# Performance work log

Measured on AMD Instinct MI355X. Metric: run time of the kernel, lower is better.

The kernel has to match this reference:

```python
import jax, jax.numpy as jnp
import numpy as np

HEADS = 20
SHIFT = 0.6931471805599453  # style_alignment_score_shift = log(2)
KEY_SCALE = 1.0             # style_alignment_score_scale
EPS = 1e-5


def expand_first(feat, scale=1.0):
    # feat: [B, H, S, D]; broadcast style features (batch items 0 and B//2)
    b = feat.shape[0]
    fs = jnp.stack([feat[0], feat[b // 2]])[:, None]           # [2,1,H,S,D]
    fs = jnp.broadcast_to(fs, (2, b // 2) + feat.shape[1:])    # [2,B/2,H,S,D]
    if scale != 1:
        fs = jnp.concatenate([fs[:, :1], scale * fs[:, 1:]], axis=1)
    return fs.reshape(feat.shape)


def concat_first(feat, scale=1.0):
    # concatenate style features along the sequence axis (-2)
    return jnp.concatenate([feat, expand_first(feat, scale=scale)], axis=-2)


def adain(feat):
    # stats over sequence axis (-2); torch .var() is unbiased (ddof=1)
    mean = feat.mean(axis=-2, keepdims=True)
    std = jnp.sqrt(feat.var(axis=-2, keepdims=True, ddof=1) + EPS)
    sm = expand_first(mean)
    ss = expand_first(std)
    return (feat - mean) / std * ss + sm


def setup_inputs() -> dict:
    key = jax.random.key(0)
    ks = jax.random.split(key, 6)
    B, S, C = 4, 1024, 1280
    sc = 1.0 / np.sqrt(C)
    return {
        "hidden_states": jax.random.normal(ks[0], (B, S, C), jnp.float32),
        "Wq": jax.random.normal(ks[1], (C, C), jnp.float32) * sc,
        "Wk": jax.random.normal(ks[2], (C, C), jnp.float32) * sc,
        "Wv": jax.random.normal(ks[3], (C, C), jnp.float32) * sc,
        "Wo": jax.random.normal(ks[4], (C, C), jnp.float32) * sc,
        "bo": jnp.zeros((C,), jnp.float32),
    }


def reference(hidden_states, Wq, Wk, Wv, Wo, bo):
    B, S, C = hidden_states.shape
    H = HEADS
    hd = C // H
    scale = hd ** -0.5

    def to_heads(t):  # [B,S,C] -> [B,H,S,hd]
        return t.reshape(B, S, H, hd).transpose(0, 2, 1, 3)

    q = to_heads(hidden_states @ Wq.T)
    k = to_heads(hidden_states @ Wk.T)
    v = to_heads(hidden_states @ Wv.T)

    q = adain(q)              # adain_queries
    k = adain(k)              # adain_keys
    # adain_values = False

    k = concat_first(k, scale=KEY_SCALE)   # [B,H,2S,hd]
    v = concat_first(v)                    # [B,H,2S,hd]

    # shifted scaled dot-product attention (shift added to shared-key block)
    logits = jnp.einsum('bhqd,bhkd->bhqk', q, k) * scale  # [B,H,S,2S]
    bias = jnp.where(jnp.arange(k.shape[-2]) >= S, jnp.float32(SHIFT), jnp.float32(0.0))
    probs = jax.nn.softmax(logits + bias, axis=-1)
    out = jnp.einsum('bhqk,bhkd->bhqd', probs, v)         # [B,H,S,hd]

    out = out.transpose(0, 2, 1, 3).reshape(B, S, C)
    out = out @ Wo.T + bo
    return out
```

## Files before the change

### kernel.cpp

```cpp
#include <hip/hip_runtime.h>
#include <math.h>


typedef __bf16 bf16x8 __attribute__((ext_vector_type(8)));
typedef __bf16 bf16x2_t __attribute__((ext_vector_type(2)));
typedef float f32x4 __attribute__((ext_vector_type(4)));
typedef unsigned short u16x8 __attribute__((ext_vector_type(8)));

#define BDIM 256

__device__ inline unsigned short f2bf(float f) {
  return __builtin_bit_cast(unsigned short, (__bf16)f);
}
__device__ inline unsigned int pack_bf2(float lo, float hi) {
  bf16x2_t v;
  v[0] = (__bf16)lo;
  v[1] = (__bf16)hi;
  return __builtin_bit_cast(unsigned int, v);
}
__device__ inline float bf2f(unsigned short h) {
  return __uint_as_float(((unsigned int)h) << 16);
}

__device__ inline void gl_lds16(const unsigned short* g, unsigned short* l) {
  __builtin_amdgcn_global_load_lds(
      (const __attribute__((address_space(1))) unsigned int*)g,
      (__attribute__((address_space(3))) unsigned int*)l, 16, 0, 0);
}

__global__ __launch_bounds__(BDIM) void k_convert_all(
    const float* __restrict__ X, const float* __restrict__ Wq,
    const float* __restrict__ Wk, const float* __restrict__ Wv,
    const float* __restrict__ Wo, unsigned short* __restrict__ Xbf,
    unsigned short* __restrict__ Wcat, unsigned short* __restrict__ Wobf) {
  const int idx = blockIdx.x * BDIM + threadIdx.x;
  const float* src;
  unsigned short* dst;
  int off;
  if (idx < 1310720) {
    src = X; dst = Xbf; off = idx;
  } else {
    const int r = idx - 1310720;
    const int which = r / 409600;
    off = r - which * 409600;
    src = (which == 0) ? Wq : (which == 1) ? Wk : (which == 2) ? Wv : Wo;
    dst = (which < 3) ? Wcat + (size_t)which * 1638400 : Wobf;
  }
  const float4 v = ((const float4*)src)[off];
  ushort4 o;
  o.x = f2bf(v.x); o.y = f2bf(v.y); o.z = f2bf(v.z); o.w = f2bf(v.w);
  ((ushort4*)dst)[off] = o;
}

__global__ __launch_bounds__(512, 1) void k_gemm_bf16(
    const unsigned short* __restrict__ A, const unsigned short* __restrict__ B,
    unsigned short* __restrict__ Cbf, int M, int N, int K) {
  __shared__ unsigned short lds[2][2][16384];

  const int bid = blockIdx.x;
  const int swz = (bid & 7) * 30 + (bid >> 3);
  const int mt = swz & 15, nt = swz >> 4;
  const int mBase = mt * 256, nBase = nt * 256;

  const int t = threadIdx.x;
  const int w = t >> 6, lane = t & 63, quad = lane >> 4, l16 = lane & 15;
  const int wrow = w & 1, wcol = w >> 1;
  const int glg = (lane & 7) ^ ((lane >> 3) & 7);
  const int NTILES = K >> 6;

  f32x4 acc[8][4];
#pragma unroll
  for (int i = 0; i < 8; ++i)
#pragma unroll
    for (int j = 0; j < 4; ++j) acc[i][j] = (f32x4){0.f, 0.f, 0.f, 0.f};

  auto stage = [&](int s, int kt) {
#pragma unroll
    for (int j = 0; j < 4; ++j) {
      const int row = j * 64 + w * 8 + (lane >> 3);
      gl_lds16(A + (size_t)(mBase + row) * K + kt * 64 + glg * 8,
               &lds[s][0][(j * 512 + w * 64 + lane) * 8]);
    }
#pragma unroll
    for (int j = 0; j < 4; ++j) {
      const int row = j * 64 + w * 8 + (lane >> 3);
      gl_lds16(B + (size_t)(nBase + row) * K + kt * 64 + glg * 8,
               &lds[s][1][(j * 512 + w * 64 + lane) * 8]);
    }
  };

  stage(0, 0);
  stage(1, 1);
  asm volatile("s_waitcnt vmcnt(8)" ::: "memory");
  __builtin_amdgcn_s_barrier();

  const int arow0 = (wrow * 128 + l16) * 64;
  const int brow0 = (wcol * 64 + l16) * 64;
  const int g0 = ((quad) ^ (l16 & 7)) * 8;
  const int g1 = ((4 + quad) ^ (l16 & 7)) * 8;

  for (int kt = 0; kt < NTILES; ++kt) {
    const int s = kt & 1;
    if (kt >= 1 && kt + 1 < NTILES) stage(s ^ 1, kt + 1);
    const unsigned short* As = &lds[s][0][0];
    const unsigned short* Bs = &lds[s][1][0];
#pragma unroll
    for (int ph = 0; ph < 4; ++ph) {
      const int mh = ph >> 1, nh = ph & 1;
      bf16x8 af[4][2], bq[2][2];
#pragma unroll
      for (int mi = 0; mi < 4; ++mi) {
        const int ro = arow0 + (mh * 4 + mi) * 1024;
        af[mi][0] = *(const bf16x8*)(As + ro + g0);
        af[mi][1] = *(const bf16x8*)(As + ro + g1);
      }
#pragma unroll
      for (int ni = 0; ni < 2; ++ni) {
        const int ro = brow0 + (nh * 2 + ni) * 1024;
        bq[ni][0] = *(const bf16x8*)(Bs + ro + g0);
        bq[ni][1] = *(const bf16x8*)(Bs + ro + g1);
      }
      __builtin_amdgcn_s_setprio(1);
#pragma unroll
      for (int kk = 0; kk < 2; ++kk)
#pragma unroll
        for (int mi = 0; mi < 4; ++mi)
#pragma unroll
          for (int ni = 0; ni < 2; ++ni)
            acc[mh * 4 + mi][nh * 2 + ni] =
                __builtin_amdgcn_mfma_f32_16x16x32_bf16(
                    af[mi][kk], bq[ni][kk], acc[mh * 4 + mi][nh * 2 + ni], 0,
                    0, 0);
      __builtin_amdgcn_s_setprio(0);
      if (ph < 3) __builtin_amdgcn_s_barrier();
    }
    asm volatile("s_waitcnt vmcnt(0)" ::: "memory");
    __builtin_amdgcn_s_barrier();
  }

#pragma unroll
  for (int mi = 0; mi < 8; ++mi)
#pragma unroll
    for (int r = 0; r < 4; ++r) {
      const int row = mBase + wrow * 128 + mi * 16 + quad * 4 + r;
#pragma unroll
      for (int ni = 0; ni < 4; ++ni)
        Cbf[(size_t)row * N + nBase + wcol * 64 + ni * 16 + l16] =
            f2bf(acc[mi][ni][r]);
    }
}

__global__ __launch_bounds__(BDIM, 2) void k_gemm_out(
    const unsigned short* __restrict__ A, const unsigned short* __restrict__ B,
    float* __restrict__ Cf, const float* __restrict__ bias, int M, int N,
    int K) {
  __shared__ unsigned short lds[2][2][8192];

  const int bid = blockIdx.x;
  const int swz = (bid & 7) * 40 + (bid >> 3);
  const int mt = swz & 31, nt = swz >> 5;
  const int mBase = mt * 128, nBase = nt * 128;

  const int t = threadIdx.x;
  const int w = t >> 6, lane = t & 63, quad = lane >> 4, l16 = lane & 15;
  const int wrow = w & 1, wcol = w >> 1;
  const int glg = (lane & 7) ^ ((lane >> 3) & 7);
  const int NTILES = K >> 6;

  f32x4 acc[4][4];
#pragma unroll
  for (int i = 0; i < 4; ++i)
#pragma unroll
    for (int j = 0; j < 4; ++j) acc[i][j] = (f32x4){0.f, 0.f, 0.f, 0.f};

  auto stage = [&](int s, int kt) {
#pragma unroll
    for (int j = 0; j < 4; ++j) {
      const int row = j * 32 + (t >> 3);
      gl_lds16(A + (size_t)(mBase + row) * K + kt * 64 + glg * 8,
               &lds[s][0][(j * 256 + t) * 8]);
    }
#pragma unroll
    for (int j = 0; j < 4; ++j) {
      const int row = j * 32 + (t >> 3);
      gl_lds16(B + (size_t)(nBase + row) * K + kt * 64 + glg * 8,
               &lds[s][1][(j * 256 + t) * 8]);
    }
  };

  stage(0, 0);
  stage(1, 1);
  asm volatile("s_waitcnt vmcnt(8)" ::: "memory");
  __builtin_amdgcn_s_barrier();

  const int arow0 = (wrow * 64 + l16) * 64;
  const int brow0 = (wcol * 64 + l16) * 64;
  const int g0 = ((quad) ^ (l16 & 7)) * 8;
  const int g1 = ((4 + quad) ^ (l16 & 7)) * 8;

  for (int kt = 0; kt < NTILES; ++kt) {
    const int s = kt & 1;
    if (kt >= 1 && kt + 1 < NTILES) stage(s ^ 1, kt + 1);
    const unsigned short* As = &lds[s][0][0];
    const unsigned short* Bs = &lds[s][1][0];
#pragma unroll
    for (int ph = 0; ph < 2; ++ph) {
      bf16x8 af[2][2], bq[4][2];
#pragma unroll
      for (int mi = 0; mi < 2; ++mi) {
        const int ro = arow0 + (ph * 2 + mi) * 1024;
        af[mi][0] = *(const bf16x8*)(As + ro + g0);
        af[mi][1] = *(const bf16x8*)(As + ro + g1);
      }
#pragma unroll
      for (int ni = 0; ni < 4; ++ni) {
        const int ro = brow0 + ni * 1024;
        bq[ni][0] = *(const bf16x8*)(Bs + ro + g0);
        bq[ni][1] = *(const bf16x8*)(Bs + ro + g1);
      }
      __builtin_amdgcn_s_setprio(1);
#pragma unroll
      for (int kk = 0; kk < 2; ++kk)
#pragma unroll
        for (int mi = 0; mi < 2; ++mi)
#pragma unroll
          for (int ni = 0; ni < 4; ++ni)
            acc[ph * 2 + mi][ni] = __builtin_amdgcn_mfma_f32_16x16x32_bf16(
                af[mi][kk], bq[ni][kk], acc[ph * 2 + mi][ni], 0, 0, 0);
      __builtin_amdgcn_s_setprio(0);
      if (ph == 0) __builtin_amdgcn_s_barrier();
    }
    asm volatile("s_waitcnt vmcnt(0)" ::: "memory");
    __builtin_amdgcn_s_barrier();
  }

#pragma unroll
  for (int mi = 0; mi < 4; ++mi)
#pragma unroll
    for (int r = 0; r < 4; ++r) {
      const int row = mBase + wrow * 64 + mi * 16 + quad * 4 + r;
#pragma unroll
      for (int ni = 0; ni < 4; ++ni) {
        const int col = nBase + wcol * 64 + ni * 16 + l16;
        Cf[(size_t)row * N + col] = acc[mi][ni][r] + bias[col];
      }
    }
}

__global__ __launch_bounds__(320) void k_stats1(
    const unsigned short* __restrict__ QKV, float* __restrict__ psum,
    float* __restrict__ psq) {
  const int z = blockIdx.y, which = z >> 2, b = z & 3;
  const int c = threadIdx.x * 4;
  const size_t base =
      (size_t)(b * 1024 + blockIdx.x * 32) * 3840 + which * 1280 + c;
  float4 s = {0.f, 0.f, 0.f, 0.f}, s2 = {0.f, 0.f, 0.f, 0.f};
#pragma unroll 8
  for (int i = 0; i < 32; ++i) {
    const ushort4 xv = *(const ushort4*)(QKV + base + (size_t)i * 3840);
    const float x0 = bf2f(xv.x), x1 = bf2f(xv.y), x2 = bf2f(xv.z),
                x3 = bf2f(xv.w);
    s.x += x0; s.y += x1; s.z += x2; s.w += x3;
    s2.x = fmaf(x0, x0, s2.x); s2.y = fmaf(x1, x1, s2.y);
    s2.z = fmaf(x2, x2, s2.z); s2.w = fmaf(x3, x3, s2.w);
  }
  const size_t o = ((size_t)z * 32 + blockIdx.x) * 1280 + c;
  *(float4*)(psum + o) = s;
  *(float4*)(psq + o) = s2;
}

__global__ __launch_bounds__(BDIM) void k_stats2(
    const float* __restrict__ psum, const float* __restrict__ psq,
    float* __restrict__ fst) {
  const int which = blockIdx.y;
  const int c = blockIdx.x * 256 + threadIdx.x;
  float m[4], sd[4];
#pragma unroll
  for (int b = 0; b < 4; ++b) {
    const int z = which * 4 + b;
    float s = 0.f, s2 = 0.f;
#pragma unroll
    for (int j = 0; j < 32; ++j) {
      s += psum[((size_t)z * 32 + j) * 1280 + c];
      s2 += psq[((size_t)z * 32 + j) * 1280 + c];
    }
    const float mean = s * (1.0f / 1024.0f);
    const float var = (s2 - 1024.0f * mean * mean) * (1.0f / 1023.0f);
    m[b] = mean;
    sd[b] = sqrtf(var + 1e-5f);
  }
  const float S2 = 0.125f * 1.44269504088896341f;
#pragma unroll
  for (int b = 0; b < 4; ++b) {
    const int bs = (b < 2) ? 0 : 2;
    const float g = sd[bs] / sd[b];
    const float o = m[bs] - m[b] * g;
    if (which == 0) {
      fst[(0 * 4 + b) * 1280 + c] = g;
      fst[(1 * 4 + b) * 1280 + c] = o;
    } else {
      fst[(2 * 4 + b) * 1280 + c] = g * S2;
      fst[(3 * 4 + b) * 1280 + c] = o;
    }
  }
}

__global__ __launch_bounds__(BDIM) void k_vt(
    const unsigned short* __restrict__ QKV, unsigned short* __restrict__ vt) {
  __shared__ unsigned short tile[64][65];
  const int tb = blockIdx.x;
  const int b = tb / 320;
  const int r2 = tb - b * 320;
  const int c0 = (r2 / 16) * 64;
  const int s0 = (r2 & 15) * 64;
  const int t = threadIdx.x;
  const int r = t >> 2, seg = (t & 3) * 16;
  const size_t goff = ((size_t)(b * 1024 + s0 + r)) * 3840 + 2560 + c0 + seg;
  const u16x8 va = *(const u16x8*)(QKV + goff);
  const u16x8 vb = *(const u16x8*)(QKV + goff + 8);
#pragma unroll
  for (int j = 0; j < 8; j++) {
    tile[r][seg + j] = va[j];
    tile[r][seg + 8 + j] = vb[j];
  }
  __syncthreads();
  u16x8 o0, o1;
#pragma unroll
  for (int j = 0; j < 8; j++) {
    o0[j] = tile[seg + j][r];
    o1[j] = tile[seg + 8 + j][r];
  }
  const size_t ooff = ((size_t)(b * 1280 + c0 + r)) * 1024 + s0 + seg;
  *(u16x8*)(vt + ooff) = o0;
  *(u16x8*)(vt + ooff + 8) = o1;
}

__global__ __launch_bounds__(BDIM, 4) void k_attn(
    const unsigned short* __restrict__ qkv, const float* __restrict__ fst,
    const unsigned short* __restrict__ vt, unsigned short* __restrict__ Op0,
    unsigned short* __restrict__ Op1, float* __restrict__ Lpart) {
  const int S = 1024;
  const int L = blockIdx.x + 8 * (blockIdx.y + 20 * blockIdx.z);
  const int qt = (L >> 3) & 7;
  const int hz = (L & 7) + ((L >> 6) << 3);
  const int h = hz % 20;
  const int zs = hz / 20;
  int b, chunk;
  if (zs < 2)      { b = 0; chunk = zs; }
  else if (zs < 6) { b = 1; chunk = zs - 2; }
  else if (zs < 8) { b = 2; chunk = zs - 6; }
  else             { b = 3; chunk = zs - 8; }
  const int ktBeg = chunk * 8;
  const int t = threadIdx.x, w = t >> 6, lane = t & 63;
  const int quad = lane >> 4, l16 = lane & 15;
  const int bstyle = (b < 2) ? 0 : 2;
  const int qrow = qt * 128 + w * 32;
  const bool style = (ktBeg >= 16);

  __shared__ unsigned short Ks[2][2][64 * 32];
  __shared__ unsigned short Vs[2][64 * 32];
  __shared__ unsigned short Plds[4][32][64];

  const float S2 = 0.125f * 1.44269504088896341f;

  bf16x8 aq[2][2];
  float biasv[2];
  {
    const int bk = style ? bstyle : b;
    float rq[2] = {0.f, 0.f};
#pragma unroll
    for (int hf = 0; hf < 2; ++hf) {
      const int cc = h * 64 + quad * 8 + hf * 32;
      float gq[8], oq[8], gs[8], ok[8];
      *(float4*)(gq)     = *(const float4*)(fst + (0 * 4 + b) * 1280 + cc);
      *(float4*)(gq + 4) = *(const float4*)(fst + (0 * 4 + b) * 1280 + cc + 4);
      *(float4*)(oq)     = *(const float4*)(fst + (1 * 4 + b) * 1280 + cc);
      *(float4*)(oq + 4) = *(const float4*)(fst + (1 * 4 + b) * 1280 + cc + 4);
      *(float4*)(gs)     = *(const float4*)(fst + (2 * 4 + bk) * 1280 + cc);
      *(float4*)(gs + 4) = *(const float4*)(fst + (2 * 4 + bk) * 1280 + cc + 4);
      *(float4*)(ok)     = *(const float4*)(fst + (3 * 4 + bk) * 1280 + cc);
      *(float4*)(ok + 4) = *(const float4*)(fst + (3 * 4 + bk) * 1280 + cc + 4);
#pragma unroll
      for (int g = 0; g < 2; ++g) {
        const size_t qoff =
            ((size_t)(b * S + qrow + g * 16 + l16)) * 3840 + cc;
        const bf16x8 qv = *(const bf16x8*)(qkv + qoff);
        bf16x8 av;
#pragma unroll
        for (int j = 0; j < 8; ++j) {
          const float qn = fmaf((float)qv[j], gq[j], oq[j]);
          rq[g] = fmaf(qn, ok[j], rq[g]);
          av[j] = (__bf16)(qn * gs[j]);
        }
        aq[g][hf] = av;
      }
    }
    const float shift = style ? 1.0f : 0.0f;
#pragma unroll
    for (int g = 0; g < 2; ++g) {
      float r = rq[g] * S2;
      r += __shfl_xor(r, 16, 64);
      r += __shfl_xor(r, 32, 64);
      biasv[g] = shift + r;
    }
  }

  bf16x8 ones;
#pragma unroll
  for (int i = 0; i < 8; ++i) ones[i] = (__bf16)1.0f;

  f32x4 o[2][4], lsum[2];
#pragma unroll
  for (int g = 0; g < 2; ++g) {
    lsum[g] = (f32x4){0.f, 0.f, 0.f, 0.f};
#pragma unroll
    for (int i = 0; i < 4; i++) o[g][i] = (f32x4){0.f, 0.f, 0.f, 0.f};
  }

  const int krow = t >> 2;
  const int kseg = ((t & 3) ^ ((t >> 3) & 3)) * 8;
  const int sw = l16 & 14;
  const int qsw = (quad ^ ((l16 >> 1) & 3)) * 8;

  auto stageK = [&](int buf, int kt) {
    const int bs = (kt < 16) ? b : bstyle;
    const int sk = (kt & 15) * 64;
    const unsigned short* kg =
        qkv + (size_t)(bs * S + sk + krow) * 3840 + 1280 + h * 64 + kseg;
    gl_lds16(kg, Ks[buf][0] + t * 8);
    gl_lds16(kg + 32, Ks[buf][1] + t * 8);
  };
  auto stageV = [&](int kt) {
    const int bs = (kt < 16) ? b : bstyle;
    const int sk = (kt & 15) * 64;
    const unsigned short* vg =
        vt + (size_t)(bs * 1280 + h * 64 + krow) * S + sk + kseg;
    gl_lds16(vg, Vs[0] + t * 8);
    gl_lds16(vg + 32, Vs[1] + t * 8);
  };

  stageK(0, ktBeg);

  for (int i = 0; i < 8; ++i) {
    const int kt = ktBeg + i;
    const int buf = i & 1;
    asm volatile("s_waitcnt vmcnt(0)" ::: "memory");
    __builtin_amdgcn_s_barrier();
    stageV(kt);
    if (i + 1 < 8) stageK(buf ^ 1, kt + 1);

    f32x4 z2[2][4];
#pragma unroll
    for (int nt = 0; nt < 4; ++nt) {
      const bf16x8 bk0 =
          *(const bf16x8*)(Ks[buf][0] + (nt * 16 + l16) * 32 + qsw);
      const bf16x8 bk1 =
          *(const bf16x8*)(Ks[buf][1] + (nt * 16 + l16) * 32 + qsw);
#pragma unroll
      for (int g = 0; g < 2; ++g) {
        f32x4 zz = (f32x4){0.f, 0.f, 0.f, 0.f};
        zz = __builtin_amdgcn_mfma_f32_16x16x32_bf16(bk0, aq[g][0], zz, 0, 0, 0);
        zz = __builtin_amdgcn_mfma_f32_16x16x32_bf16(bk1, aq[g][1], zz, 0, 0, 0);
        z2[g][nt] = zz;
      }
    }

#pragma unroll
    for (int g = 0; g < 2; ++g) {
      const float bg = biasv[g];
#pragma unroll
      for (int nt = 0; nt < 4; ++nt) {
        const float e0 = exp2f(z2[g][nt][0] + bg);
        const float e1 = exp2f(z2[g][nt][1] + bg);
        const float e2 = exp2f(z2[g][nt][2] + bg);
        const float e3 = exp2f(z2[g][nt][3] + bg);
        uint2 pk;
        pk.x = pack_bf2(e0, e1);
        pk.y = pack_bf2(e2, e3);
        const int phys = (nt * 4 + quad) ^ sw;
        *(uint2*)(&Plds[w][g * 16 + l16][phys * 4]) = pk;
      }
    }

    if (i + 1 < 8)
      asm volatile("s_waitcnt vmcnt(2)" ::: "memory");
    else
      asm volatile("s_waitcnt vmcnt(0)" ::: "memory");
    __builtin_amdgcn_s_barrier();

#pragma unroll
    for (int g = 0; g < 2; ++g) {
      const int a0 = (2 * quad) ^ sw;
      const int a1 = (2 * quad + 8) ^ sw;
      const bf16x8 pa0 = *(const bf16x8*)(&Plds[w][g * 16 + l16][a0 * 4]);
      const bf16x8 pa1 = *(const bf16x8*)(&Plds[w][g * 16 + l16][a1 * 4]);
      lsum[g] = __builtin_amdgcn_mfma_f32_16x16x32_bf16(pa0, ones, lsum[g], 0, 0, 0);
      lsum[g] = __builtin_amdgcn_mfma_f32_16x16x32_bf16(pa1, ones, lsum[g], 0, 0, 0);
#pragma unroll
      for (int dt = 0; dt < 4; ++dt) {
        const bf16x8 vb0 =
            *(const bf16x8*)(Vs[0] + (dt * 16 + l16) * 32 + qsw);
        const bf16x8 vb1 =
            *(const bf16x8*)(Vs[1] + (dt * 16 + l16) * 32 + qsw);
        o[g][dt] =
            __builtin_amdgcn_mfma_f32_16x16x32_bf16(pa0, vb0, o[g][dt], 0, 0, 0);
        o[g][dt] =
            __builtin_amdgcn_mfma_f32_16x16x32_bf16(pa1, vb1, o[g][dt], 0, 0, 0);
      }
    }
  }

  if (l16 == 0) {
#pragma unroll
    for (int g = 0; g < 2; ++g)
#pragma unroll
      for (int r = 0; r < 4; ++r)
        Lpart[((size_t)zs * 20 + h) * 1024 + qrow + g * 16 + quad * 4 + r] =
            lsum[g][r];
  }

  unsigned short* Op = (zs < 4) ? Op0 + (size_t)zs * 1310720
                                : Op1 + (size_t)(zs - 4) * 1310720;
#pragma unroll
  for (int g = 0; g < 2; ++g)
#pragma unroll
    for (int dt = 0; dt < 4; ++dt)
#pragma unroll
      for (int r = 0; r < 4; ++r)
        Op[(size_t)(qrow + g * 16 + quad * 4 + r) * 1280 + h * 64 + dt * 16 +
           l16] = f2bf(o[g][dt][r]);
}

__global__ __launch_bounds__(BDIM) void k_combine(
    const unsigned short* __restrict__ Op0, const unsigned short* __restrict__ Op1,
    const float* __restrict__ Lpart, unsigned short* __restrict__ attnb) {
  const int idx = blockIdx.x * BDIM + threadIdx.x;
  const int row = idx / 160;
  const int c = (idx - row * 160) * 8;
  const int b = row >> 10, q = row & 1023, h = c >> 6;
  const int zb = (b >> 1) * 6 + (b & 1) * 2;
  const int ns = 2 + (b & 1) * 2;
  float L = 0.f;
  float acc[8] = {0.f, 0.f, 0.f, 0.f, 0.f, 0.f, 0.f, 0.f};
  for (int s = 0; s < ns; ++s) {
    const int z = zb + s;
    const unsigned short* base = (z < 4)
        ? Op0 + (size_t)z * 1310720
        : Op1 + (size_t)(z - 4) * 1310720;
    L += Lpart[((size_t)z * 20 + h) * 1024 + q];
    const u16x8 v = *(const u16x8*)(base + (size_t)q * 1280 + c);
#pragma unroll
    for (int j = 0; j < 8; ++j) acc[j] += bf2f(v[j]);
  }
  const float rl = 1.0f / L;
  u16x8 o8;
#pragma unroll
  for (int j = 0; j < 8; ++j) o8[j] = f2bf(acc[j] * rl);
  *(u16x8*)(attnb + (size_t)row * 1280 + c) = o8;
}

extern "C" void kernel_launch(void* const* d_in, const int* in_sizes, int n_in,
                              void* d_out, int out_size, void* d_ws,
                              size_t ws_size, hipStream_t stream) {
  const float* X = (const float*)d_in[0];
  const float* Wq = (const float*)d_in[1];
  const float* Wk = (const float*)d_in[2];
  const float* Wv = (const float*)d_in[3];
  const float* Wo = (const float*)d_in[4];
  const float* bo = (const float*)d_in[5];
  float* out = (float*)d_out;

  char* ws = (char*)d_ws;
  size_t off = 0;
  auto alloc = [&](size_t bytes) {
    char* p = ws + off;
    off += (bytes + 255) & ~(size_t)255;
    return p;
  };
  unsigned short* Wcat = (unsigned short*)alloc(3840ull * 1280 * 2);
  unsigned short* Xbf = (unsigned short*)alloc(4096ull * 1280 * 2);
  unsigned short* QKV = (unsigned short*)alloc(4096ull * 3840 * 2);
  unsigned short* Wobf = (unsigned short*)alloc(1280ull * 1280 * 2);
  float* fstats = (float*)alloc(4ull * 4 * 1280 * 4);
  unsigned short* qnb = (unsigned short*)alloc(4096ull * 1280 * 2);
  unsigned short* knb = (unsigned short*)alloc(4096ull * 1280 * 2);
  unsigned short* vtb = (unsigned short*)alloc(4096ull * 1280 * 2);
  unsigned short* attnb = (unsigned short*)alloc(4096ull * 1280 * 2);
  (void)knb;

  unsigned short* Op0 = Xbf;
  unsigned short* Op1 = qnb;
  float* Lpart = (float*)Wcat;
  float* psum = (float*)attnb;
  float* psq = (float*)(attnb + 4096ull * 1280 / 2);

  k_convert_all<<<11520, BDIM, 0, stream>>>(X, Wq, Wk, Wv, Wo, Xbf, Wcat, Wobf);
  k_gemm_bf16<<<240, 512, 0, stream>>>(Xbf, Wcat, QKV, 4096, 3840, 1280);
  k_stats1<<<dim3(32, 8), 320, 0, stream>>>(QKV, psum, psq);
  k_stats2<<<dim3(5, 2), BDIM, 0, stream>>>(psum, psq, fstats);
  k_vt<<<1280, BDIM, 0, stream>>>(QKV, vtb);
  k_attn<<<dim3(8, 20, 12), BDIM, 0, stream>>>(QKV, fstats, vtb, Op0, Op1,
                                               Lpart);
  k_combine<<<2560, BDIM, 0, stream>>>(Op0, Op1, Lpart, attnb);
  k_gemm_out<<<320, BDIM, 0, stream>>>(attnb, Wobf, out, bo, 4096, 1280, 1280);
}
```

Baseline: 247.3 us.

## Switch both GEMMs to 4-stage K=32 LDS ring with one barrier per step

```diff
diff --git a/kernel.cpp b/kernel.cpp
--- a/kernel.cpp
+++ b/kernel.cpp
@@ -55,7 +55,7 @@
 __global__ __launch_bounds__(512, 1) void k_gemm_bf16(
     const unsigned short* __restrict__ A, const unsigned short* __restrict__ B,
     unsigned short* __restrict__ Cbf, int M, int N, int K) {
-  __shared__ unsigned short lds[2][2][16384];
+  __shared__ unsigned short lds[4][2][256 * 32];
 
   const int bid = blockIdx.x;
   const int swz = (bid & 7) * 30 + (bid >> 3);
@@ -65,8 +65,7 @@
   const int t = threadIdx.x;
   const int w = t >> 6, lane = t & 63, quad = lane >> 4, l16 = lane & 15;
   const int wrow = w & 1, wcol = w >> 1;
-  const int glg = (lane & 7) ^ ((lane >> 3) & 7);
-  const int NTILES = K >> 6;
+  const int NTILES = K >> 5;
 
   f32x4 acc[8][4];
 #pragma unroll
@@ -74,68 +73,60 @@
 #pragma unroll
     for (int j = 0; j < 4; ++j) acc[i][j] = (f32x4){0.f, 0.f, 0.f, 0.f};
 
+  const int srow = t >> 2;
+  const int sgl = ((t & 3) ^ ((t >> 3) & 3)) * 8;
+
   auto stage = [&](int s, int kt) {
 #pragma unroll
-    for (int j = 0; j < 4; ++j) {
-      const int row = j * 64 + w * 8 + (lane >> 3);
-      gl_lds16(A + (size_t)(mBase + row) * K + kt * 64 + glg * 8,
-               &lds[s][0][(j * 512 + w * 64 + lane) * 8]);
-    }
-#pragma unroll
-    for (int j = 0; j < 4; ++j) {
-      const int row = j * 64 + w * 8 + (lane >> 3);
-      gl_lds16(B + (size_t)(nBase + row) * K + kt * 64 + glg * 8,
-               &lds[s][1][(j * 512 + w * 64 + lane) * 8]);
+    for (int j = 0; j < 2; ++j) {
+      const int row = j * 128 + srow;
+      gl_lds16(A + (size_t)(mBase + row) * K + kt * 32 + sgl,
+               &lds[s][0][(j * 512 + t) * 8]);
+    }
+#pragma unroll
+    for (int j = 0; j < 2; ++j) {
+      const int row = j * 128 + srow;
+      gl_lds16(B + (size_t)(nBase + row) * K + kt * 32 + sgl,
+               &lds[s][1][(j * 512 + t) * 8]);
     }
   };
 
   stage(0, 0);
   stage(1, 1);
-  asm volatile("s_waitcnt vmcnt(8)" ::: "memory");
-  __builtin_amdgcn_s_barrier();
-
-  const int arow0 = (wrow * 128 + l16) * 64;
-  const int brow0 = (wcol * 64 + l16) * 64;
-  const int g0 = ((quad) ^ (l16 & 7)) * 8;
-  const int g1 = ((4 + quad) ^ (l16 & 7)) * 8;
+
+  const int arow0 = (wrow * 128 + l16) * 32;
+  const int brow0 = (wcol * 64 + l16) * 32;
+  const int gsw = (quad ^ ((l16 >> 1) & 3)) * 8;
 
   for (int kt = 0; kt < NTILES; ++kt) {
-    const int s = kt & 1;
-    if (kt >= 1 && kt + 1 < NTILES) stage(s ^ 1, kt + 1);
+    const int s = kt & 3;
+    if (kt + 2 < NTILES) {
+      stage((kt + 2) & 3, kt + 2);
+      asm volatile("s_waitcnt vmcnt(8)" ::: "memory");
+    } else if (kt + 1 < NTILES) {
+      asm volatile("s_waitcnt vmcnt(4)" ::: "memory");
+    } else {
+      asm volatile("s_waitcnt vmcnt(0)" ::: "memory");
+    }
+    __builtin_amdgcn_s_barrier();
+
     const unsigned short* As = &lds[s][0][0];
     const unsigned short* Bs = &lds[s][1][0];
-#pragma unroll
-    for (int ph = 0; ph < 4; ++ph) {
-      const int mh = ph >> 1, nh = ph & 1;
-      bf16x8 af[4][2], bq[2][2];
-#pragma unroll
-      for (int mi = 0; mi < 4; ++mi) {
-        const int ro = arow0 + (mh * 4 + mi) * 1024;
-        af[mi][0] = *(const bf16x8*)(As + ro + g0);
-        af[mi][1] = *(const bf16x8*)(As + ro + g1);
-      }
-#pragma unroll
-      for (int ni = 0; ni < 2; ++ni) {
-        const int ro = brow0 + (nh * 2 + ni) * 1024;
-        bq[ni][0] = *(const bf16x8*)(Bs + ro + g0);
-        bq[ni][1] = *(const bf16x8*)(Bs + ro + g1);
-      }
-      __builtin_amdgcn_s_setprio(1);
-#pragma unroll
-      for (int kk = 0; kk < 2; ++kk)
-#pragma unroll
-        for (int mi = 0; mi < 4; ++mi)
-#pragma unroll
-          for (int ni = 0; ni < 2; ++ni)
-            acc[mh * 4 + mi][nh * 2 + ni] =
-                __builtin_amdgcn_mfma_f32_16x16x32_bf16(
-                    af[mi][kk], bq[ni][kk], acc[mh * 4 + mi][nh * 2 + ni], 0,
-                    0, 0);
-      __builtin_amdgcn_s_setprio(0);
-      if (ph < 3) __builtin_amdgcn_s_barrier();
-    }
-    asm volatile("s_waitcnt vmcnt(0)" ::: "memory");
-    __builtin_amdgcn_s_barrier();
+    bf16x8 af[8], bq[4];
+#pragma unroll
+    for (int mi = 0; mi < 8; ++mi)
+      af[mi] = *(const bf16x8*)(As + arow0 + mi * 512 + gsw);
+#pragma unroll
+    for (int ni = 0; ni < 4; ++ni)
+      bq[ni] = *(const bf16x8*)(Bs + brow0 + ni * 512 + gsw);
+    __builtin_amdgcn_s_setprio(1);
+#pragma unroll
+    for (int mi = 0; mi < 8; ++mi)
+#pragma unroll
+      for (int ni = 0; ni < 4; ++ni)
+        acc[mi][ni] = __builtin_amdgcn_mfma_f32_16x16x32_bf16(
+            af[mi], bq[ni], acc[mi][ni], 0, 0, 0);
+    __builtin_amdgcn_s_setprio(0);
   }
 
 #pragma unroll
@@ -154,7 +145,7 @@
     const unsigned short* __restrict__ A, const unsigned short* __restrict__ B,
     float* __restrict__ Cf, const float* __restrict__ bias, int M, int N,
     int K) {
-  __shared__ unsigned short lds[2][2][8192];
+  __shared__ unsigned short lds[4][2][128 * 32];
 
   const int bid = blockIdx.x;
   const int swz = (bid & 7) * 40 + (bid >> 3);
@@ -164,8 +155,7 @@
   const int t = threadIdx.x;
   const int w = t >> 6, lane = t & 63, quad = lane >> 4, l16 = lane & 15;
   const int wrow = w & 1, wcol = w >> 1;
-  const int glg = (lane & 7) ^ ((lane >> 3) & 7);
-  const int NTILES = K >> 6;
+  const int NTILES = K >> 5;
 
   f32x4 acc[4][4];
 #pragma unroll
@@ -173,65 +163,60 @@
 #pragma unroll
     for (int j = 0; j < 4; ++j) acc[i][j] = (f32x4){0.f, 0.f, 0.f, 0.f};
 
+  const int srow = t >> 2;
+  const int sgl = ((t & 3) ^ ((t >> 3) & 3)) * 8;
+
   auto stage = [&](int s, int kt) {
 #pragma unroll
-    for (int j = 0; j < 4; ++j) {
-      const int row = j * 32 + (t >> 3);
-      gl_lds16(A + (size_t)(mBase + row) * K + kt * 64 + glg * 8,
+    for (int j = 0; j < 2; ++j) {
+      const int row = j * 64 + srow;
+      gl_lds16(A + (size_t)(mBase + row) * K + kt * 32 + sgl,
                &lds[s][0][(j * 256 + t) * 8]);
     }
 #pragma unroll
-    for (int j = 0; j < 4; ++j) {
-      const int row = j * 32 + (t >> 3);
-      gl_lds16(B + (size_t)(nBase + row) * K + kt * 64 + glg * 8,
+    for (int j = 0; j < 2; ++j) {
+      const int row = j * 64 + srow;
+      gl_lds16(B + (size_t)(nBase + row) * K + kt * 32 + sgl,
                &lds[s][1][(j * 256 + t) * 8]);
     }
   };
 
   stage(0, 0);
   stage(1, 1);
-  asm volatile("s_waitcnt vmcnt(8)" ::: "memory");
-  __builtin_amdgcn_s_barrier();
-
-  const int arow0 = (wrow * 64 + l16) * 64;
-  const int brow0 = (wcol * 64 + l16) * 64;
-  const int g0 = ((quad) ^ (l16 & 7)) * 8;
-  const int g1 = ((4 + quad) ^ (l16 & 7)) * 8;
+
+  const int arow0 = (wrow * 64 + l16) * 32;
+  const int brow0 = (wcol * 64 + l16) * 32;
+  const int gsw = (quad ^ ((l16 >> 1) & 3)) * 8;
 
   for (int kt = 0; kt < NTILES; ++kt) {
-    const int s = kt & 1;
-    if (kt >= 1 && kt + 1 < NTILES) stage(s ^ 1, kt + 1);
+    const int s = kt & 3;
+    if (kt + 2 < NTILES) {
+      stage((kt + 2) & 3, kt + 2);
+      asm volatile("s_waitcnt vmcnt(8)" ::: "memory");
+    } else if (kt + 1 < NTILES) {
+      asm volatile("s_waitcnt vmcnt(4)" ::: "memory");
+    } else {
+      asm volatile("s_waitcnt vmcnt(0)" ::: "memory");
+    }
+    __builtin_amdgcn_s_barrier();
+
     const unsigned short* As = &lds[s][0][0];
     const unsigned short* Bs = &lds[s][1][0];
-#pragma unroll
-    for (int ph = 0; ph < 2; ++ph) {
-      bf16x8 af[2][2], bq[4][2];
-#pragma unroll
-      for (int mi = 0; mi < 2; ++mi) {
-        const int ro = arow0 + (ph * 2 + mi) * 1024;
-        af[mi][0] = *(const bf16x8*)(As + ro + g0);
-        af[mi][1] = *(const bf16x8*)(As + ro + g1);
-      }
-#pragma unroll
-      for (int ni = 0; ni < 4; ++ni) {
-        const int ro = brow0 + ni * 1024;
-        bq[ni][0] = *(const bf16x8*)(Bs + ro + g0);
-        bq[ni][1] = *(const bf16x8*)(Bs + ro + g1);
-      }
-      __builtin_amdgcn_s_setprio(1);
-#pragma unroll
-      for (int kk = 0; kk < 2; ++kk)
-#pragma unroll
-        for (int mi = 0; mi < 2; ++mi)
-#pragma unroll
-          for (int ni = 0; ni < 4; ++ni)
-            acc[ph * 2 + mi][ni] = __builtin_amdgcn_mfma_f32_16x16x32_bf16(
-                af[mi][kk], bq[ni][kk], acc[ph * 2 + mi][ni], 0, 0, 0);
-      __builtin_amdgcn_s_setprio(0);
-      if (ph == 0) __builtin_amdgcn_s_barrier();
-    }
-    asm volatile("s_waitcnt vmcnt(0)" ::: "memory");
-    __builtin_amdgcn_s_barrier();
+    bf16x8 af[4], bq[4];
+#pragma unroll
+    for (int mi = 0; mi < 4; ++mi)
+      af[mi] = *(const bf16x8*)(As + arow0 + mi * 512 + gsw);
+#pragma unroll
+    for (int ni = 0; ni < 4; ++ni)
+      bq[ni] = *(const bf16x8*)(Bs + brow0 + ni * 512 + gsw);
+    __builtin_amdgcn_s_setprio(1);
+#pragma unroll
+    for (int mi = 0; mi < 4; ++mi)
+#pragma unroll
+      for (int ni = 0; ni < 4; ++ni)
+        acc[mi][ni] = __builtin_amdgcn_mfma_f32_16x16x32_bf16(
+            af[mi], bq[ni], acc[mi][ni], 0, 0, 0);
+    __builtin_amdgcn_s_setprio(0);
   }
 
 #pragma unroll
```

After: 246.2 us. About the same (-0.4%).
